# Kernel tuning notes

Hardware: AMD Instinct MI355X
Metric: run time of the kernel (lower is better)

Reference implementation:

```python
import jax, jax.numpy as jnp
import numpy as np

B, N, D = 4, 2048, 1024
THRESHOLD_FACTOR = 1.25


def setup_inputs() -> dict:
    key = jax.random.key(0)
    ks = jax.random.split(key, 8)
    s = 0.02  # init scale matching torch.randn * 0.02
    return {
        "hidden_states": jax.random.normal(ks[0], (B, N, D), jnp.float32),
        "Wq": jax.random.normal(ks[1], (D, D), jnp.float32) * s,
        "bq": jnp.zeros((D,), jnp.float32),
        "Wk": jax.random.normal(ks[2], (D, D), jnp.float32) * s,
        "bk": jnp.zeros((D,), jnp.float32),
        "Wv": jax.random.normal(ks[3], (D, D), jnp.float32) * s,
        "bv": jnp.zeros((D,), jnp.float32),
        "Wo": jax.random.normal(ks[4], (D, D), jnp.float32) * s,
        "bo": jnp.zeros((D,), jnp.float32),
        "Wtq": jax.random.normal(ks[5], (2, D), jnp.float32) * s,  # nn.Linear(D, 2)
        "btq": jnp.zeros((2,), jnp.float32),
        "Wfq": jax.random.normal(ks[6], (D, 2), jnp.float32) * s,  # HebbianLinear(2, D)
        "bfq": jnp.zeros((D,), jnp.float32),
    }


def _linear(x, W, b):
    return x @ W.T + b


def reference(hidden_states, Wq, bq, Wk, bk, Wv, bv, Wo, bo, Wtq, btq, Wfq, bfq):
    d = hidden_states.shape[-1]
    q = _linear(hidden_states, Wq, bq)
    k = _linear(hidden_states, Wk, bk)
    v = _linear(hidden_states, Wv, bv)
    scores = jnp.einsum('bid,bjd->bij', q, k) / jnp.sqrt(jnp.asarray(d, scores_dtype := q.dtype))

    # PhaseAwareBinaryAttention on 2-d quantum projection
    qp = _linear(hidden_states, Wtq, btq)            # [B, N, 2]
    diff = qp[:, :, None, :] - qp[:, None, :, :]      # [B, N, N, 2]
    dist_sq = jnp.sum(diff * diff, axis=-1)           # [B, N, N]
    phase_diff = jnp.arctan2(diff[..., 1], diff[..., 0])
    forward_bias = 0.5 * (1.0 + jnp.cos(phase_diff))
    mean_dist = jnp.mean(dist_sq, axis=(-1, -2), keepdims=True)
    std_dist = jnp.std(dist_sq, axis=(-1, -2), keepdims=True, ddof=1)  # torch unbiased std
    threshold = mean_dist + THRESHOLD_FACTOR * std_dist
    n = dist_sq.shape[-1]
    causal = jnp.tril(jnp.ones((n, n), bool))
    valid = (dist_sq <= threshold) & causal[None]
    binary_attn = valid.astype(scores.dtype) * forward_bias

    masked = jnp.where(binary_attn == 0, -jnp.inf, scores)
    weights = jax.nn.softmax(masked, axis=-1)
    context = jnp.einsum('bij,bjd->bid', weights, v)
    output = _linear(context, Wo, bo)

    # F.normalize(qp, p=2, dim=-1) with eps=1e-12
    r_embed = qp / jnp.maximum(jnp.linalg.norm(qp, axis=-1, keepdims=True), 1e-12)
    quantum_output = _linear(r_embed, Wfq, bfq)
    return hidden_states + output + 0.1 * quantum_output
```

## Files before the change

kernel.cpp:

```cpp
#include <hip/hip_runtime.h>
#include <math.h>

#define N_TOK 2048
#define DIM   1024
#define BATCH 4

typedef float v4f  __attribute__((ext_vector_type(4)));
typedef __bf16 v8bf __attribute__((ext_vector_type(8)));
typedef unsigned short v8us __attribute__((ext_vector_type(8)));

static __device__ __forceinline__ unsigned short f2bf(float f) {
  unsigned int u = __float_as_uint(f);
  u += 0x7fffu + ((u >> 16) & 1u);
  return (unsigned short)(u >> 16);
}
static __device__ __forceinline__ float bf2f(unsigned short h) {
  return __uint_as_float((unsigned int)h << 16);
}

__global__ __launch_bounds__(256) void castqp_kernel(
    const float* __restrict__ hs, const float* __restrict__ Wtq,
    const float* __restrict__ btq, unsigned short* __restrict__ hs_b,
    float2* __restrict__ qp, float2* __restrict__ remb) {
  int w = threadIdx.x >> 6, lane = threadIdx.x & 63;
  int row = blockIdx.x * 4 + w;
  const float* x = hs + (size_t)row * DIM;
  unsigned short* d = hs_b + (size_t)row * DIM;
  float a0 = 0.f, a1 = 0.f;
#pragma unroll
  for (int it = 0; it < 4; ++it) {
    int base = it * 256 + lane * 4;
    float4 v = *(const float4*)(x + base);
    float4 w0 = *(const float4*)(Wtq + base);
    float4 w1 = *(const float4*)(Wtq + DIM + base);
    ushort4 pk;
    pk.x = f2bf(v.x); pk.y = f2bf(v.y); pk.z = f2bf(v.z); pk.w = f2bf(v.w);
    *(ushort4*)(d + base) = pk;
    a0 += v.x * w0.x + v.y * w0.y + v.z * w0.z + v.w * w0.w;
    a1 += v.x * w1.x + v.y * w1.y + v.z * w1.z + v.w * w1.w;
  }
  for (int o = 32; o; o >>= 1) { a0 += __shfl_xor(a0, o); a1 += __shfl_xor(a1, o); }
  if (lane == 0) {
    a0 += btq[0]; a1 += btq[1];
    qp[row] = make_float2(a0, a1);
    float nrm = fmaxf(sqrtf(a0 * a0 + a1 * a1), 1e-12f);
    remb[row] = make_float2(a0 / nrm, a1 / nrm);
  }
}

__global__ __launch_bounds__(256) void cast_w4_kernel(
    const float* __restrict__ W0, const float* __restrict__ W1,
    const float* __restrict__ W2, const float* __restrict__ W3,
    unsigned short* __restrict__ D0, unsigned short* __restrict__ D1,
    unsigned short* __restrict__ D2, unsigned short* __restrict__ D3) {
  const float* s;
  unsigned short* d;
  switch (blockIdx.y) {
    case 0: s = W0; d = D0; break;
    case 1: s = W1; d = D1; break;
    case 2: s = W2; d = D2; break;
    default: s = W3; d = D3; break;
  }
  int i = (blockIdx.x * 256 + threadIdx.x) * 4;
  float4 v = *(const float4*)(s + i);
  d[i + 0] = f2bf(v.x); d[i + 1] = f2bf(v.y);
  d[i + 2] = f2bf(v.z); d[i + 3] = f2bf(v.w);
}

__global__ __launch_bounds__(256) void moments_kernel(
    const float2* __restrict__ qp, double* __restrict__ part) {
  int b = blockIdx.y;
  int i0 = blockIdx.x * 32;
  const float2* qb = qp + ((size_t)b << 11);
  double s1 = 0.0, s2 = 0.0;
  for (int idx = threadIdx.x; idx < 32 * N_TOK; idx += 256) {
    int i = i0 + (idx >> 11), j = idx & (N_TOK - 1);
    float2 pi = qb[i], pj = qb[j];
    float dx = pi.x - pj.x, dy = pi.y - pj.y;
    float dd = __fadd_rn(__fmul_rn(dx, dx), __fmul_rn(dy, dy));
    s1 += (double)dd;
    s2 += (double)dd * (double)dd;
  }
  int lane = threadIdx.x & 63, w = threadIdx.x >> 6;
  for (int o = 32; o; o >>= 1) { s1 += __shfl_xor(s1, o); s2 += __shfl_xor(s2, o); }
  __shared__ double red[8];
  if (lane == 0) { red[w] = s1; red[4 + w] = s2; }
  __syncthreads();
  if (threadIdx.x == 0) {
    int slot = b * 64 + blockIdx.x;
    part[slot * 2 + 0] = red[0] + red[1] + red[2] + red[3];
    part[slot * 2 + 1] = red[4] + red[5] + red[6] + red[7];
  }
}

__global__ __launch_bounds__(256) void thr_kernel(
    const double* __restrict__ part, float* __restrict__ thr) {
  int b = threadIdx.x >> 6, lane = threadIdx.x & 63;
  double s1 = part[(b * 64 + lane) * 2 + 0];
  double s2 = part[(b * 64 + lane) * 2 + 1];
  for (int o = 32; o; o >>= 1) { s1 += __shfl_xor(s1, o); s2 += __shfl_xor(s2, o); }
  if (lane == 0) {
    double n2 = (double)N_TOK * (double)N_TOK;
    double mean = s1 / n2;
    double var = (s2 - n2 * mean * mean) / (n2 - 1.0);
    if (var < 0.0) var = 0.0;
    thr[b] = (float)(mean + 1.25 * sqrt(var));
  }
}

template<int NFRAG>
__device__ __forceinline__ void gemm_ktile_loopN(
    const unsigned short* __restrict__ Ag, const unsigned short* __restrict__ Bg,
    int ldA, int ldB, int kEnd,
    unsigned short* As, unsigned short* Bs, v4f acc[4][NFRAG]) {
  const int tid  = threadIdx.x;
  const int lane = tid & 63;
  const int wm   = ((tid >> 6) & 1) << 6;
  const int wn   = (tid >> 7) * (NFRAG * 16);
  const int quad = lane >> 4, l16 = lane & 15;
  const int srow = tid >> 3;
  const int scol = ((tid ^ srow) & 7) * 8;
  for (int k0 = 0; k0 < kEnd; k0 += 64) {
    __syncthreads();
#pragma unroll
    for (int it = 0; it < 4; ++it) {
      const unsigned short* ga = Ag + (size_t)(srow + it * 32) * ldA + k0 + scol;
      unsigned short* la = As + (size_t)(it * 256 + (tid & ~63)) * 8;
      __builtin_amdgcn_global_load_lds((const __attribute__((address_space(1))) void*)ga,
                                       (__attribute__((address_space(3))) void*)la, 16, 0, 0);
    }
#pragma unroll
    for (int it = 0; it < NFRAG; ++it) {
      const unsigned short* gb = Bg + (size_t)(srow + it * 32) * ldB + k0 + scol;
      unsigned short* lb = Bs + (size_t)(it * 256 + (tid & ~63)) * 8;
      __builtin_amdgcn_global_load_lds((const __attribute__((address_space(1))) void*)gb,
                                       (__attribute__((address_space(3))) void*)lb, 16, 0, 0);
    }
    asm volatile("s_waitcnt vmcnt(0)" ::: "memory");
    __syncthreads();
#pragma unroll
    for (int kk = 0; kk < 64; kk += 32) {
      const int co = ((((kk >> 3) + quad) ^ (l16 & 7)) << 3);
      v8bf af[4], bfv[NFRAG];
#pragma unroll
      for (int i = 0; i < 4; ++i)
        af[i] = *(const v8bf*)(As + (wm + i * 16 + l16) * 64 + co);
#pragma unroll
      for (int i = 0; i < NFRAG; ++i)
        bfv[i] = *(const v8bf*)(Bs + (wn + i * 16 + l16) * 64 + co);
#pragma unroll
      for (int mi = 0; mi < 4; ++mi)
#pragma unroll
        for (int ni = 0; ni < NFRAG; ++ni)
          acc[mi][ni] = __builtin_amdgcn_mfma_f32_16x16x32_bf16(af[mi], bfv[ni], acc[mi][ni], 0, 0, 0);
    }
  }
}

#define PROLOG128                                                     \
  __shared__ __attribute__((aligned(16))) unsigned short smem[2][128 * 64];\
  unsigned short* As = smem[0];                                       \
  unsigned short* Bs = smem[1];                                       \
  v4f acc[4][4];                                                      \
  _Pragma("unroll") for (int i_ = 0; i_ < 4; ++i_)                    \
  _Pragma("unroll") for (int j_ = 0; j_ < 4; ++j_)                    \
      acc[i_][j_] = v4f{0.f, 0.f, 0.f, 0.f};                          \
  const int lane = threadIdx.x & 63, w = threadIdx.x >> 6;            \
  const int wm = (w & 1) << 6, wn = (w >> 1) << 6;                    \
  const int quad = lane >> 4, l16 = lane & 15;

#define PROLOG12864                                                   \
  __shared__ __attribute__((aligned(16))) unsigned short As[128 * 64];\
  __shared__ __attribute__((aligned(16))) unsigned short Bs[64 * 64]; \
  v4f acc[4][2];                                                      \
  _Pragma("unroll") for (int i_ = 0; i_ < 4; ++i_)                    \
  _Pragma("unroll") for (int j_ = 0; j_ < 2; ++j_)                    \
      acc[i_][j_] = v4f{0.f, 0.f, 0.f, 0.f};                          \
  const int lane = threadIdx.x & 63, w = threadIdx.x >> 6;            \
  const int wm = (w & 1) << 6, wn = (w >> 1) << 5;                    \
  const int quad = lane >> 4, l16 = lane & 15;

__global__ __launch_bounds__(256) void gemm_qkv_fused_kernel(
    const unsigned short* __restrict__ X, const unsigned short* __restrict__ Wqkv,
    const float* __restrict__ bq, const float* __restrict__ bk,
    const float* __restrict__ bv, unsigned short* __restrict__ q_b,
    unsigned short* __restrict__ k_b, unsigned short* __restrict__ v_t) {
  PROLOG128
  int lid = blockIdx.y * 24 + blockIdx.x;
  int xcd = lid & 7, slot = lid >> 3;
  int by = (xcd << 3) | (slot & 7);
  int bx = slot >> 3;
  int m0 = by * 128, n0 = bx * 128;
  gemm_ktile_loopN<4>(X + (size_t)m0 * DIM, Wqkv + (size_t)n0 * DIM, DIM, DIM, DIM, As, Bs, acc);
  int region = n0 >> 10;
  const float* bias = region == 0 ? bq : region == 1 ? bk : bv;
  int cbase = n0 & 1023;
  if (region < 2) {
    unsigned short* dst = region == 0 ? q_b : k_b;
#pragma unroll
    for (int mi = 0; mi < 4; ++mi) {
      int row0 = m0 + wm + mi * 16 + quad * 4;
#pragma unroll
      for (int ni = 0; ni < 4; ++ni) {
        int col = cbase + wn + ni * 16 + l16;
        float bcol = bias[col];
#pragma unroll
        for (int r = 0; r < 4; ++r)
          dst[(size_t)(row0 + r) * DIM + col] = f2bf(acc[mi][ni][r] + bcol);
      }
    }
  } else {
    unsigned short* T = &smem[0][0];
    __syncthreads();
#pragma unroll
    for (int mi = 0; mi < 4; ++mi) {
      int trow = wm + mi * 16 + quad * 4;
#pragma unroll
      for (int ni = 0; ni < 4; ++ni) {
        int fcol = wn + ni * 16 + l16;
        float bcol = bias[cbase + fcol];
        ushort4 pk;
        pk.x = f2bf(acc[mi][ni][0] + bcol);
        pk.y = f2bf(acc[mi][ni][1] + bcol);
        pk.z = f2bf(acc[mi][ni][2] + bcol);
        pk.w = f2bf(acc[mi][ni][3] + bcol);
        *(ushort4*)(T + fcol * 128 + trow) = pk;
      }
    }
    __syncthreads();
    int bb = m0 >> 11, tok0 = m0 & (N_TOK - 1);
    unsigned short* dstb = v_t + ((size_t)(bb << 10) + cbase) * N_TOK + tok0;
#pragma unroll
    for (int kk2 = 0; kk2 < 8; ++kk2) {
      int c = kk2 * 256 + threadIdx.x;
      int f = c >> 4, e0 = (c & 15) * 8;
      v8us v = *(const v8us*)(T + f * 128 + e0);
      *(v8us*)(dstb + (size_t)f * N_TOK + e0) = v;
    }
  }
}

__global__ __launch_bounds__(256) void gemm_scores_kernel(
    const unsigned short* __restrict__ q, const unsigned short* __restrict__ k,
    const float2* __restrict__ qp, const float* __restrict__ thr,
    unsigned short* __restrict__ S) {
  PROLOG12864
  int b = blockIdx.y;
  int lid = blockIdx.x;
  int t = (lid & 7) * 34 + (lid >> 3);
  int ti = (int)((sqrtf(4.f * (float)t + 1.f) - 1.f) * 0.5f);
  while ((ti + 1) * (ti + 2) <= t) ++ti;
  while (ti * (ti + 1) > t) --ti;
  int tj = t - ti * (ti + 1);
  int i0 = ti * 128, j0 = tj * 64;
  const unsigned short* qb = q + (size_t)b * N_TOK * DIM;
  const unsigned short* kb = k + (size_t)b * N_TOK * DIM;
  gemm_ktile_loopN<2>(qb + (size_t)i0 * DIM, kb + (size_t)j0 * DIM, DIM, DIM, DIM,
                      As, Bs, acc);
  float th = thr[b];
  const float2* qpb = qp + ((size_t)b << 11);
  unsigned short* Sb = S + (size_t)b * N_TOK * N_TOK;
  float2 pjv[2];
#pragma unroll
  for (int ni = 0; ni < 2; ++ni) pjv[ni] = qpb[j0 + wn + ni * 16 + l16];
#pragma unroll
  for (int mi = 0; mi < 4; ++mi) {
#pragma unroll
    for (int r = 0; r < 4; ++r) {
      int i = i0 + wm + mi * 16 + quad * 4 + r;
      float2 pi2 = qpb[i];
#pragma unroll
      for (int ni = 0; ni < 2; ++ni) {
        int j = j0 + wn + ni * 16 + l16;
        if (j <= i) {
          float dx = pi2.x - pjv[ni].x, dy = pi2.y - pjv[ni].y;
          float dd = __fadd_rn(__fmul_rn(dx, dx), __fmul_rn(dy, dy));
          bool ok = (dd <= th);
          if (ok && dx < 0.f && fabsf(dy) <= 3e-4f * (-dx)) {
            float fb = 0.5f * (1.f + cosf(atan2f(dy, dx)));
            if (fb == 0.f) ok = false;
          }
          Sb[(size_t)i * N_TOK + j] = ok ? f2bf(acc[mi][ni][r] * 0.03125f) : 0xFF80;
        }
      }
    }
  }
}

__global__ __launch_bounds__(256) void softmax_kernel(
    const unsigned short* __restrict__ S, unsigned short* __restrict__ P) {
  int row = blockIdx.x;
  int b = row >> 11, i = row & (N_TOK - 1);
  const unsigned short* s = S + ((size_t)b * N_TOK + i) * N_TOK;
  unsigned short* p = P + ((size_t)b * N_TOK + i) * N_TOK;
  int tid = threadIdx.x, lane = tid & 63, w = tid >> 6;
  int lim = i + 1;
  int tail0 = lim & ~7, ntail = lim - tail0;
  __shared__ float redmax[4], redsum[4];
  float mx = -__builtin_inff();
  for (int j = tid * 8; j + 8 <= lim; j += 2048) {
    v8us v = *(const v8us*)(s + j);
#pragma unroll
    for (int e = 0; e < 8; ++e) mx = fmaxf(mx, bf2f(v[e]));
  }
  if (tid < ntail) mx = fmaxf(mx, bf2f(s[tail0 + tid]));
  for (int o = 32; o; o >>= 1) mx = fmaxf(mx, __shfl_xor(mx, o));
  if (lane == 0) redmax[w] = mx;
  __syncthreads();
  mx = fmaxf(fmaxf(redmax[0], redmax[1]), fmaxf(redmax[2], redmax[3]));
  float sum = 0.f;
  for (int j = tid * 8; j + 8 <= lim; j += 2048) {
    v8us v = *(const v8us*)(s + j);
#pragma unroll
    for (int e = 0; e < 8; ++e) sum += __expf(bf2f(v[e]) - mx);
  }
  if (tid < ntail) sum += __expf(bf2f(s[tail0 + tid]) - mx);
  for (int o = 32; o; o >>= 1) sum += __shfl_xor(sum, o);
  if (lane == 0) redsum[w] = sum;
  __syncthreads();
  sum = redsum[0] + redsum[1] + redsum[2] + redsum[3];
  float inv = 1.f / sum;
  for (int j = tid * 8; j + 8 <= lim; j += 2048) {
    v8us v = *(const v8us*)(s + j);
    v8us o;
#pragma unroll
    for (int e = 0; e < 8; ++e) o[e] = f2bf(__expf(bf2f(v[e]) - mx) * inv);
    *(v8us*)(p + j) = o;
  }
  if (tid < ntail) p[tail0 + tid] = f2bf(__expf(bf2f(s[tail0 + tid]) - mx) * inv);
  int zs = (lim + 7) & ~7;
  if (tid < zs - lim) p[lim + tid] = 0;
  v8us zv;
#pragma unroll
  for (int e = 0; e < 8; ++e) zv[e] = 0;
  for (int j = zs + tid * 8; j < N_TOK; j += 2048) *(v8us*)(p + j) = zv;
}

__global__ __launch_bounds__(256) void gemm_pv_kernel(
    const unsigned short* __restrict__ P, const unsigned short* __restrict__ vt,
    unsigned short* __restrict__ ctx) {
  PROLOG12864
  int b = blockIdx.z;
  int ti = 15 - blockIdx.y;
  int d0 = blockIdx.x * 64;
  int i0 = ti * 128;
  const unsigned short* Pb = P + (size_t)b * N_TOK * N_TOK;
  const unsigned short* Vb = vt + ((size_t)b * DIM + d0) * N_TOK;
  int kEnd = (ti + 1) * 128;
  gemm_ktile_loopN<2>(Pb + (size_t)i0 * N_TOK, Vb, N_TOK, N_TOK, kEnd,
                      As, Bs, acc);
#pragma unroll
  for (int mi = 0; mi < 4; ++mi) {
    int row0 = i0 + wm + mi * 16 + quad * 4;
#pragma unroll
    for (int ni = 0; ni < 2; ++ni) {
      int d = d0 + wn + ni * 16 + l16;
#pragma unroll
      for (int r = 0; r < 4; ++r)
        ctx[((size_t)b * N_TOK + row0 + r) * DIM + d] = f2bf(acc[mi][ni][r]);
    }
  }
}

__global__ __launch_bounds__(256) void gemm_out_kernel(
    const unsigned short* __restrict__ ctx, const unsigned short* __restrict__ Wob,
    const float* __restrict__ bo, const float* __restrict__ hs,
    const float2* __restrict__ remb, const float* __restrict__ Wfq,
    const float* __restrict__ bfq, float* __restrict__ out) {
  PROLOG12864
  int lid = blockIdx.y * 16 + blockIdx.x;
  int xcd = lid & 7, slot = lid >> 3;
  int by = (xcd << 3) | (slot & 7);
  int bx = slot >> 3;
  int m0 = by * 128, n0 = bx * 64;
  gemm_ktile_loopN<2>(ctx + (size_t)m0 * DIM, Wob + (size_t)n0 * DIM, DIM, DIM, DIM,
                      As, Bs, acc);
#pragma unroll
  for (int mi = 0; mi < 4; ++mi) {
    int row0 = m0 + wm + mi * 16 + quad * 4;
#pragma unroll
    for (int ni = 0; ni < 2; ++ni) {
      int col = n0 + wn + ni * 16 + l16;
      float bias2 = bo[col] + 0.1f * bfq[col];
      float wf0 = 0.1f * Wfq[col * 2 + 0], wf1 = 0.1f * Wfq[col * 2 + 1];
#pragma unroll
      for (int r = 0; r < 4; ++r) {
        int row = row0 + r;
        float2 re = remb[row];
        out[(size_t)row * DIM + col] =
            acc[mi][ni][r] + bias2 + hs[(size_t)row * DIM + col] + re.x * wf0 + re.y * wf1;
      }
    }
  }
}

extern "C" void kernel_launch(void* const* d_in, const int* in_sizes, int n_in,
                              void* d_out, int out_size, void* d_ws, size_t ws_size,
                              hipStream_t stream) {
  const float* hs  = (const float*)d_in[0];
  const float* Wq  = (const float*)d_in[1];
  const float* bq  = (const float*)d_in[2];
  const float* Wk  = (const float*)d_in[3];
  const float* bk  = (const float*)d_in[4];
  const float* Wv  = (const float*)d_in[5];
  const float* bv  = (const float*)d_in[6];
  const float* Wo  = (const float*)d_in[7];
  const float* bo  = (const float*)d_in[8];
  const float* Wtq = (const float*)d_in[9];
  const float* btq = (const float*)d_in[10];
  const float* Wfq = (const float*)d_in[11];
  const float* bfq = (const float*)d_in[12];
  float* out = (float*)d_out;

  char* ws = (char*)d_ws;
  size_t off = 0;
  auto alloc = [&](size_t bytes) {
    char* p = ws + off;
    off += (bytes + 255) & ~(size_t)255;
    return p;
  };
  unsigned short* hs_b = (unsigned short*)alloc((size_t)8192 * 1024 * 2);
  unsigned short* q_b  = (unsigned short*)alloc((size_t)8192 * 1024 * 2);
  unsigned short* k_b  = (unsigned short*)alloc((size_t)8192 * 1024 * 2);
  unsigned short* v_t  = (unsigned short*)alloc((size_t)8192 * 1024 * 2);
  unsigned short* Wq_b = (unsigned short*)alloc((size_t)1024 * 1024 * 2);
  unsigned short* Wk_b = (unsigned short*)alloc((size_t)1024 * 1024 * 2);
  unsigned short* Wv_b = (unsigned short*)alloc((size_t)1024 * 1024 * 2);
  unsigned short* Wo_b = (unsigned short*)alloc((size_t)1024 * 1024 * 2);
  float2* qp   = (float2*)alloc((size_t)8192 * 8);
  float2* remb = (float2*)alloc((size_t)8192 * 8);
  double* part = (double*)alloc((size_t)BATCH * 64 * 2 * 8);
  float*  thr  = (float*)alloc(64);
  unsigned short* S = (unsigned short*)alloc((size_t)BATCH * N_TOK * N_TOK * 2);
  unsigned short* P   = q_b;
  unsigned short* ctx = hs_b;

  castqp_kernel<<<2048, 256, 0, stream>>>(hs, Wtq, btq, hs_b, qp, remb);
  cast_w4_kernel<<<dim3(1024, 4), 256, 0, stream>>>(Wq, Wk, Wv, Wo, Wq_b, Wk_b, Wv_b, Wo_b);
  moments_kernel<<<dim3(64, BATCH), 256, 0, stream>>>((const float2*)qp, part);
  thr_kernel<<<1, 256, 0, stream>>>(part, thr);

  gemm_qkv_fused_kernel<<<dim3(24, 64), 256, 0, stream>>>(
      hs_b, Wq_b, bq, bk, bv, q_b, k_b, v_t);

  gemm_scores_kernel<<<dim3(272, 4), 256, 0, stream>>>(
      q_b, k_b, (const float2*)qp, thr, S);

  softmax_kernel<<<8192, 256, 0, stream>>>(S, P);

  gemm_pv_kernel<<<dim3(16, 16, 4), 256, 0, stream>>>(P, v_t, ctx);

  gemm_out_kernel<<<dim3(16, 64), 256, 0, stream>>>(ctx, Wo_b, bo, hs, remb, Wfq, bfq, out);
}
```

Before: 338.9 us.

## Double-buffer LDS tiles with async global_load_lds in 128x64 GEMMs

```diff
diff --git a/kernel.cpp b/kernel.cpp
--- a/kernel.cpp
+++ b/kernel.cpp
@@ -157,6 +157,84 @@
   }
 }
 
+#define SBAR asm volatile("s_barrier" ::: "memory")
+
+__device__ __forceinline__ void compute_12864(
+    const unsigned short* As, const unsigned short* Bs,
+    int wm, int wn, int quad, int l16, v4f acc[4][2]) {
+#pragma unroll
+  for (int kk = 0; kk < 64; kk += 32) {
+    const int co = ((((kk >> 3) + quad) ^ (l16 & 7)) << 3);
+    v8bf af[4], bfv[2];
+#pragma unroll
+    for (int i = 0; i < 4; ++i)
+      af[i] = *(const v8bf*)(As + (wm + i * 16 + l16) * 64 + co);
+#pragma unroll
+    for (int i = 0; i < 2; ++i)
+      bfv[i] = *(const v8bf*)(Bs + (wn + i * 16 + l16) * 64 + co);
+#pragma unroll
+    for (int mi = 0; mi < 4; ++mi)
+#pragma unroll
+      for (int ni = 0; ni < 2; ++ni)
+        acc[mi][ni] = __builtin_amdgcn_mfma_f32_16x16x32_bf16(af[mi], bfv[ni], acc[mi][ni], 0, 0, 0);
+  }
+}
+
+__device__ __forceinline__ void gemm_ktile_loop64_cnt(
+    const unsigned short* __restrict__ Ag, const unsigned short* __restrict__ Bg,
+    int ldA, int ldB, int kEnd,
+    unsigned short* As0, unsigned short* Bs0,
+    unsigned short* As1, unsigned short* Bs1, v4f acc[4][2]) {
+  const int tid  = threadIdx.x;
+  const int lane = tid & 63;
+  const int wm   = ((tid >> 6) & 1) << 6;
+  const int wn   = (tid >> 7) << 5;
+  const int quad = lane >> 4, l16 = lane & 15;
+  const int srow = tid >> 3;
+  const int scol = ((tid ^ srow) & 7) * 8;
+  const unsigned short* gA = Ag + (size_t)srow * ldA + scol;
+  const unsigned short* gB = Bg + (size_t)srow * ldB + scol;
+  const int lbase = (tid & ~63) * 8;
+
+  auto stage = [&](unsigned short* As, unsigned short* Bs, int k0) {
+#pragma unroll
+    for (int it = 0; it < 4; ++it) {
+      const unsigned short* ga = gA + (size_t)(it * 32) * ldA + k0;
+      __builtin_amdgcn_global_load_lds((const __attribute__((address_space(1))) void*)ga,
+                                       (__attribute__((address_space(3))) void*)(As + it * 2048 + lbase), 16, 0, 0);
+    }
+#pragma unroll
+    for (int it = 0; it < 2; ++it) {
+      const unsigned short* gb = gB + (size_t)(it * 32) * ldB + k0;
+      __builtin_amdgcn_global_load_lds((const __attribute__((address_space(1))) void*)gb,
+                                       (__attribute__((address_space(3))) void*)(Bs + it * 2048 + lbase), 16, 0, 0);
+    }
+  };
+
+  stage(As0, Bs0, 0);
+  stage(As1, Bs1, 64);
+  int k0 = 0;
+  for (; k0 + 128 < kEnd; k0 += 128) {
+    asm volatile("s_waitcnt vmcnt(6)" ::: "memory");
+    SBAR;
+    compute_12864(As0, Bs0, wm, wn, quad, l16, acc);
+    SBAR;
+    stage(As0, Bs0, k0 + 128);
+    asm volatile("s_waitcnt vmcnt(6)" ::: "memory");
+    SBAR;
+    compute_12864(As1, Bs1, wm, wn, quad, l16, acc);
+    SBAR;
+    stage(As1, Bs1, k0 + 192);
+  }
+  asm volatile("s_waitcnt vmcnt(6)" ::: "memory");
+  SBAR;
+  compute_12864(As0, Bs0, wm, wn, quad, l16, acc);
+  SBAR;
+  asm volatile("s_waitcnt vmcnt(0)" ::: "memory");
+  SBAR;
+  compute_12864(As1, Bs1, wm, wn, quad, l16, acc);
+}
+
 #define PROLOG128                                                     \
   __shared__ __attribute__((aligned(16))) unsigned short smem[2][128 * 64];\
   unsigned short* As = smem[0];                                       \
@@ -169,9 +247,9 @@
   const int wm = (w & 1) << 6, wn = (w >> 1) << 6;                    \
   const int quad = lane >> 4, l16 = lane & 15;
 
-#define PROLOG12864                                                   \
-  __shared__ __attribute__((aligned(16))) unsigned short As[128 * 64];\
-  __shared__ __attribute__((aligned(16))) unsigned short Bs[64 * 64]; \
+#define PROLOG12864DB                                                 \
+  __shared__ __attribute__((aligned(16))) unsigned short Asm[2][128 * 64];\
+  __shared__ __attribute__((aligned(16))) unsigned short Bsm[2][64 * 64]; \
   v4f acc[4][2];                                                      \
   _Pragma("unroll") for (int i_ = 0; i_ < 4; ++i_)                    \
   _Pragma("unroll") for (int j_ = 0; j_ < 2; ++j_)                    \
@@ -244,7 +322,7 @@
     const unsigned short* __restrict__ q, const unsigned short* __restrict__ k,
     const float2* __restrict__ qp, const float* __restrict__ thr,
     unsigned short* __restrict__ S) {
-  PROLOG12864
+  PROLOG12864DB
   int b = blockIdx.y;
   int lid = blockIdx.x;
   int t = (lid & 7) * 34 + (lid >> 3);
@@ -255,8 +333,8 @@
   int i0 = ti * 128, j0 = tj * 64;
   const unsigned short* qb = q + (size_t)b * N_TOK * DIM;
   const unsigned short* kb = k + (size_t)b * N_TOK * DIM;
-  gemm_ktile_loopN<2>(qb + (size_t)i0 * DIM, kb + (size_t)j0 * DIM, DIM, DIM, DIM,
-                      As, Bs, acc);
+  gemm_ktile_loop64_cnt(qb + (size_t)i0 * DIM, kb + (size_t)j0 * DIM, DIM, DIM, DIM,
+                        Asm[0], Bsm[0], Asm[1], Bsm[1], acc);
   float th = thr[b];
   const float2* qpb = qp + ((size_t)b << 11);
   unsigned short* Sb = S + (size_t)b * N_TOK * N_TOK;
@@ -330,16 +408,17 @@
   if (tid < ntail) p[tail0 + tid] = f2bf(__expf(bf2f(s[tail0 + tid]) - mx) * inv);
   int zs = (lim + 7) & ~7;
   if (tid < zs - lim) p[lim + tid] = 0;
+  int rend = (lim + 127) & ~127;
   v8us zv;
 #pragma unroll
   for (int e = 0; e < 8; ++e) zv[e] = 0;
-  for (int j = zs + tid * 8; j < N_TOK; j += 2048) *(v8us*)(p + j) = zv;
+  for (int j = zs + tid * 8; j < rend; j += 2048) *(v8us*)(p + j) = zv;
 }
 
 __global__ __launch_bounds__(256) void gemm_pv_kernel(
     const unsigned short* __restrict__ P, const unsigned short* __restrict__ vt,
     unsigned short* __restrict__ ctx) {
-  PROLOG12864
+  PROLOG12864DB
   int b = blockIdx.z;
   int ti = 15 - blockIdx.y;
   int d0 = blockIdx.x * 64;
@@ -347,8 +426,8 @@
   const unsigned short* Pb = P + (size_t)b * N_TOK * N_TOK;
   const unsigned short* Vb = vt + ((size_t)b * DIM + d0) * N_TOK;
   int kEnd = (ti + 1) * 128;
-  gemm_ktile_loopN<2>(Pb + (size_t)i0 * N_TOK, Vb, N_TOK, N_TOK, kEnd,
-                      As, Bs, acc);
+  gemm_ktile_loop64_cnt(Pb + (size_t)i0 * N_TOK, Vb, N_TOK, N_TOK, kEnd,
+                        Asm[0], Bsm[0], Asm[1], Bsm[1], acc);
 #pragma unroll
   for (int mi = 0; mi < 4; ++mi) {
     int row0 = i0 + wm + mi * 16 + quad * 4;
@@ -367,14 +446,14 @@
     const float* __restrict__ bo, const float* __restrict__ hs,
     const float2* __restrict__ remb, const float* __restrict__ Wfq,
     const float* __restrict__ bfq, float* __restrict__ out) {
-  PROLOG12864
+  PROLOG12864DB
   int lid = blockIdx.y * 16 + blockIdx.x;
   int xcd = lid & 7, slot = lid >> 3;
   int by = (xcd << 3) | (slot & 7);
   int bx = slot >> 3;
   int m0 = by * 128, n0 = bx * 64;
-  gemm_ktile_loopN<2>(ctx + (size_t)m0 * DIM, Wob + (size_t)n0 * DIM, DIM, DIM, DIM,
-                      As, Bs, acc);
+  gemm_ktile_loop64_cnt(ctx + (size_t)m0 * DIM, Wob + (size_t)n0 * DIM, DIM, DIM, DIM,
+                        Asm[0], Bsm[0], Asm[1], Bsm[1], acc);
 #pragma unroll
   for (int mi = 0; mi < 4; ++mi) {
     int row0 = m0 + wm + mi * 16 + quad * 4;
```

After: 332.5 us. About the same (-1.9%).
